# Kernel optimization log

Measured on AMD Instinct MI355X. Metric: run time of the kernel, lower is better.

The kernel has to match this reference:

```python
import jax, jax.numpy as jnp
import numpy as np

K = 16        # max_points
S = 3         # num_scales
D_MODEL = 256
KDIM = 16
TAU = 1e-4
B_BATCH = 512


def _boundaries(k):
    edges = [(i, j) for i in range(k) for j in range(i + 1, k)]
    tris = [(i, j, kk) for i in range(k) for j in range(i + 1, k) for kk in range(j + 1, k)]
    E, T = len(edges), len(tris)
    B1 = np.zeros((k, E), np.float32)
    for e, (i, j) in enumerate(edges):
        B1[i, e] = -1.0
        B1[j, e] = 1.0
    e2i = {e: idx for idx, e in enumerate(edges)}
    B2 = np.zeros((E, T), np.float32)
    for t, (i, j, kk) in enumerate(tris):
        B2[e2i[(j, kk)], t] = 1.0
        B2[e2i[(i, kk)], t] = -1.0
        B2[e2i[(i, j)], t] = 1.0
    e_i = np.array([e[0] for e in edges], np.int32)
    e_j = np.array([e[1] for e in edges], np.int32)
    t_ij = np.array([e2i[(a, b)] for (a, b, c) in tris], np.int32)
    t_jk = np.array([e2i[(b, c)] for (a, b, c) in tris], np.int32)
    t_ik = np.array([e2i[(a, c)] for (a, b, c) in tris], np.int32)
    return B1, B2, e_i, e_j, t_ij, t_jk, t_ik


def setup_inputs() -> dict:
    key = jax.random.key(0)
    ks = jax.random.split(key, 8)
    d = D_MODEL
    B1, B2, e_i, e_j, t_ij, t_jk, t_ik = _boundaries(K)

    def lin(kk, fin, fout):
        return jax.random.normal(kk, (fin, fout), jnp.float32) / np.sqrt(fin).astype(np.float32)

    return dict(
        x=jax.random.normal(ks[0], (B_BATCH, K, d), jnp.float32),
        mask=jnp.ones((B_BATCH, K), jnp.float32),
        B1=jnp.asarray(B1), B2=jnp.asarray(B2), abs_B1=jnp.asarray(np.abs(B1)),
        e_i=jnp.asarray(e_i), e_j=jnp.asarray(e_j),
        t_ij=jnp.asarray(t_ij), t_jk=jnp.asarray(t_jk), t_ik=jnp.asarray(t_ik),
        log_scales=jnp.linspace(-1.5, 1.5, S).astype(jnp.float32),
        Wg=lin(ks[1], d, KDIM), bg=jnp.zeros((KDIM,), jnp.float32),
        Wv0=lin(ks[2], d, d * S), bv0=jnp.zeros((d * S,), jnp.float32),
        We=lin(ks[3], d, d * S), be=jnp.zeros((d * S,), jnp.float32),
        Wout=lin(ks[4], 2 * S * d, d), bout=jnp.zeros((d,), jnp.float32),
        g1=jnp.ones((d,), jnp.float32), b1=jnp.zeros((d,), jnp.float32),
        g2=jnp.ones((d,), jnp.float32), b2=jnp.zeros((d,), jnp.float32),
        Wf1=lin(ks[5], d, 4 * d), bf1=jnp.zeros((4 * d,), jnp.float32),
        Wf2=lin(ks[6], 4 * d, d), bf2=jnp.zeros((d,), jnp.float32),
    )


def _layernorm(x, g, b):
    mu = jnp.mean(x, -1, keepdims=True)
    var = jnp.mean(jnp.square(x - mu), -1, keepdims=True)
    return (x - mu) * jax.lax.rsqrt(var + 1e-5) * g + b


def _forward(x, mask, B1, B2, abs_B1, e_i, e_j, t_ij, t_jk, t_ik,
             log_scales, Wg, bg, Wv0, bv0, We, be, Wout, bout,
             g1, b1, g2, b2, Wf1, bf1, Wf2, bf2):
    B, Kp, d = x.shape
    E = B1.shape[1]
    residual = x
    x_norm = _layernorm(x, g1, b1)
    P = x_norm @ Wg + bg                                   # (B,K,k_dim)
    mask2 = mask[:, :, None] * mask[:, None, :]            # (B,K,K)
    # cdist (safe sqrt: zero diag, no NaN grads)
    pn = jnp.sum(P * P, -1)
    d2 = jnp.maximum(pn[:, :, None] + pn[:, None, :] - 2.0 * jnp.einsum('bik,bjk->bij', P, P), 0.0)
    Dm = jnp.where(d2 > 0, jnp.sqrt(jnp.where(d2 > 0, d2, 1.0)), 0.0) * mask2
    sigma_sq = jnp.square(jnp.exp(log_scales))             # (S,)
    A = jnp.exp(-(Dm * Dm)[:, None] / (2.0 * sigma_sq[None, :, None, None] + 1e-8)) * mask2[:, None]  # (B,S,K,K)
    W1 = A[:, :, e_i, e_j]                                 # (B,S,E) edge gather
    W2 = W1[:, :, t_ij] * W1[:, :, t_jk] * W1[:, :, t_ik]  # (B,S,T) triangle weights
    V0 = (x_norm @ Wv0 + bv0).reshape(B, Kp, S, d).transpose(0, 2, 1, 3)         # (B,S,K,d)
    E_raw = jnp.einsum('ke,bkd->bed', abs_B1, x_norm)                            # (B,E,d)
    E_in = (E_raw @ We + be).reshape(B, E, S, d).transpose(0, 2, 1, 3)           # (B,S,E,d)
    # L0 = B1 diag(W1) B1^T + tau I
    L0 = jnp.einsum('ke,bse,me->bskm', B1, W1, B1) + TAU * jnp.eye(Kp, dtype=x.dtype)
    M0 = jnp.einsum('bskm,bsmd->bskd', L0, V0)
    # L1 = B1^T diag(mask) B1 + B2 diag(W2) B2^T + tau I
    term_down = jnp.einsum('ke,bk,kf->bef', B1, mask, B1)                        # (B,E,E)
    term_up = jnp.einsum('et,bst,ft->bsef', B2, W2, B2)                          # (B,S,E,E)
    L1 = term_down[:, None] + term_up + TAU * jnp.eye(E, dtype=x.dtype)
    M1 = jnp.einsum('bsef,bsfd->bsed', L1, E_in)
    M1n = jnp.einsum('ke,bsed->bskd', abs_B1, M1)                                # edges -> nodes
    node_cat = M0.transpose(0, 2, 1, 3).reshape(B, Kp, S * d)
    edge_cat = M1n.transpose(0, 2, 1, 3).reshape(B, Kp, S * d)
    attn = jnp.concatenate([node_cat, edge_cat], -1) @ Wout + bout
    x2 = residual + attn                                   # dropout is identity in eval
    h = jax.nn.gelu(_layernorm(x2, g2, b2) @ Wf1 + bf1, approximate=False) @ Wf2 + bf2
    return x2 + h


def reference(x, mask, B1, B2, abs_B1, e_i, e_j, t_ij, t_jk, t_ik,
              log_scales, Wg, bg, Wv0, bv0, We, be, Wout, bout,
              g1, b1, g2, b2, Wf1, bf1, Wf2, bf2):
    return _forward(x, mask, B1, B2, abs_B1, e_i, e_j, t_ij, t_jk, t_ik,
                    log_scales, Wg, bg, Wv0, bv0, We, be, Wout, bout,
                    g1, b1, g2, b2, Wf1, bf1, Wf2, bf2)
```

## Files before the change

kernel.cpp:

```cpp
#include <hip/hip_runtime.h>
#include <math.h>

#define KN 16
#define DM 256
#define NS 3
#define NE 120
#define NT_TRI 560
#define NBATCH 512
#define TAUF 1e-4f
#define KAUG 1664

typedef unsigned short ushort_t;
typedef __attribute__((ext_vector_type(8))) short short8v;
typedef __attribute__((ext_vector_type(4))) short short4v;
typedef __attribute__((ext_vector_type(4))) float f32x4;

#define OFF_WSTACK 0u
#define OFF_WF1T   851968u
#define OFF_WF2T   1376256u
#define OFF_TOPO   1900544u
#define OFF_RST    1908736u
#define OFF_TBF    2105344u
#define OFF_XNT    5251072u
#define OFF_Z      13639680u
#define OFF_H      13639680u

__device__ __forceinline__ ushort_t f2bf(float f) {
    union { float f; unsigned int u; } v; v.f = f;
    unsigned int r = v.u + 0x7FFFu + ((v.u >> 16) & 1u);
    return (ushort_t)(r >> 16);
}
__device__ __forceinline__ void gload_lds16(const void* g, void* l) {
    auto gp = (const __attribute__((address_space(1))) unsigned int*)(unsigned long long)(g);
    auto lp = (__attribute__((address_space(3))) unsigned int*)(unsigned long long)(l);
    __builtin_amdgcn_global_load_lds(gp, lp, 16, 0, 0);
}

__global__ __launch_bounds__(256) void prep_kernel(
    const float* __restrict__ Wv0, const float* __restrict__ bv0,
    const float* __restrict__ We,  const float* __restrict__ be,
    const float* __restrict__ Wout,
    const float* __restrict__ Wf1, const float* __restrict__ Wf2,
    const int* __restrict__ e_i, const int* __restrict__ e_j,
    const int* __restrict__ t_ij, const int* __restrict__ t_jk, const int* __restrict__ t_ik,
    ushort_t* __restrict__ wstack, ushort_t* __restrict__ wf1t,
    ushort_t* __restrict__ wf2t,
    float* __restrict__ topoF, int* __restrict__ midOff, int* __restrict__ triSrt)
{
    __shared__ float lhs[16][DM];
    __shared__ float tile[64][65];
    __shared__ int   eidxL[256];
    __shared__ int   eiL[NE], ejL[NE];
    __shared__ int   midL[NT_TRI], pkL[NT_TRI];
    __shared__ int   cnts[16], offs[17];
    const int bid = blockIdx.x;
    const int j = threadIdx.x;

    if (bid == 230) {
        eidxL[j] = -1;
        if (j < NE) { eiL[j] = e_i[j]; ejL[j] = e_j[j]; }
        __syncthreads();
        if (j < NE) {
            eidxL[eiL[j]*16 + ejL[j]] = j;
            eidxL[ejL[j]*16 + eiL[j]] = j;
        }
        __syncthreads();
        const int n = j >> 4, m = j & 15;
        float q, p2, adj;
        if (n != m) {
            const int e = eidxL[j];
            if (e >= 0) { q = (m == ejL[e]) ? 1.f : -1.f; p2 = 1.f; adj = 1.f; }
            else        { q = 0.f; p2 = 0.f; adj = 0.f; }
        } else {
            q = 0.f; p2 = 0.f; adj = 0.f;
            for (int kk = 0; kk < KN; ++kk) {
                if (kk == n) continue;
                const int e = eidxL[n*16 + kk];
                if (e >= 0) { q += (n == ejL[e]) ? 1.f : -1.f; p2 += 1.f; }
            }
        }
        topoF[j] = q; topoF[256 + j] = p2; topoF[512 + j] = adj;

        for (int tt = j; tt < NT_TRI; tt += 256) {
            const int eij = t_ij[tt], ejk = t_jk[tt], eik = t_ik[tt];
            const int a0 = eiL[eij], a1 = ejL[eij];
            const int b0 = eiL[ejk], b1v = ejL[ejk];
            const int c0 = eiL[eik], c1 = ejL[eik];
            const int mid = (b0 == a0 || b0 == a1) ? b0 : b1v;
            midL[tt] = mid;
            pkL[tt]  = (a0*16 + a1) | ((b0*16 + b1v) << 8) | ((c0*16 + c1) << 16);
        }
        __syncthreads();
        if (j < 16) {
            int c = 0;
            for (int tt = 0; tt < NT_TRI; ++tt) c += (midL[tt] == j);
            cnts[j] = c;
        }
        __syncthreads();
        if (j == 0) {
            int s = 0;
            for (int q2 = 0; q2 < 16; ++q2) { offs[q2] = s; s += cnts[q2]; }
            offs[16] = s;
        }
        __syncthreads();
        if (j < 17) midOff[j] = offs[j];
        for (int tt = j; tt < NT_TRI; tt += 256) {
            const int mid = midL[tt];
            int r = 0;
            for (int q2 = 0; q2 < NT_TRI; ++q2)
                r += (q2 < tt && midL[q2] == mid);
            triSrt[offs[mid] + r] = pkL[tt];
        }
        return;
    }

    if (bid < 102) {
        const int m = bid / 17, by = bid % 17;
        const int path = m / 3, s = m % 3;
        const float* __restrict__ Wo = Wout + (size_t)m*DM*DM;
        if (by == 16) {
            const float* bv = (path == 0) ? bv0 : be;
            const float f = (path == 0) ? 1.0f : 0.5f;
            float acc = 0.f;
            for (int k = 0; k < DM; ++k)
                acc += bv[s*DM + k] * f * Wo[k*DM + j];
            wstack[(size_t)j*KAUG + 1536 + m] = f2bf(acc);
            if (m == 0)
                for (int c = 1542; c < KAUG; ++c)
                    wstack[(size_t)j*KAUG + c] = 0;
            return;
        }
        const float* src = (path == 0) ? Wv0 : We;
        const int i0 = by * 16;
        for (int r = 0; r < 16; ++r)
            lhs[r][j] = src[(size_t)(i0 + r)*(NS*DM) + s*DM + j];
        __syncthreads();
        float acc[16];
#pragma unroll
        for (int r = 0; r < 16; ++r) acc[r] = 0.f;
        for (int k = 0; k < DM; ++k) {
            const float w = Wo[k*DM + j];
#pragma unroll
            for (int r = 0; r < 16; ++r) acc[r] += lhs[r][k] * w;
        }
#pragma unroll
        for (int r = 0; r < 16; ++r)
            wstack[(size_t)j*KAUG + m*DM + i0 + r] = f2bf(acc[r]);
        return;
    }

    const float* in; ushort_t* outp; int R, C, rt, ct;
    if (bid < 166) {
        const int q = bid - 102;
        in = Wf1; outp = wf1t; R = 256; C = 1024;
        rt = (q >> 4) * 64; ct = (q & 15) * 64;
    } else {
        const int q = bid - 166;
        in = Wf2; outp = wf2t; R = 1024; C = 256;
        rt = (q >> 2) * 64; ct = (q & 3) * 64;
    }
#pragma unroll
    for (int q2 = 0; q2 < 16; ++q2) {
        const int idx = q2*256 + j;
        const int r = idx >> 6, c = idx & 63;
        tile[r][c] = in[(size_t)(rt + r)*C + ct + c];
    }
    __syncthreads();
#pragma unroll
    for (int q2 = 0; q2 < 16; ++q2) {
        const int idx = q2*256 + j;
        const int cc = idx >> 6, rr = idx & 63;
        outp[(size_t)(ct + cc)*R + rt + rr] = f2bf(tile[rr][cc]);
    }
}

__global__ __launch_bounds__(256) void topo_kernel(
    const float* __restrict__ x, const float* __restrict__ mask,
    const float* __restrict__ log_scales,
    const float* __restrict__ Wg, const float* __restrict__ bg,
    const float* __restrict__ g1, const float* __restrict__ b1,
    const float* __restrict__ topoF, const int* __restrict__ midOff,
    const int* __restrict__ triSrt,
    ushort_t* __restrict__ tbf, ushort_t* __restrict__ xnt,
    float* __restrict__ rstOut)
{
    const int b = blockIdx.x;
    const int t = threadIdx.x;
    const int n = t >> 4, m = t & 15;

    __shared__ ushort_t xnbT[DM][32];
    __shared__ float Plds[KN][KN];
    __shared__ float mskL[KN];
    __shared__ float QL[256];
    __shared__ float P2L[256];
    __shared__ float adjL[256];
    __shared__ float sA[NS][KN][KN];
    __shared__ float part[4][NS][KN];
    __shared__ ushort_t Tbf[6][KN][32];

    QL[t]  = topoF[t];
    P2L[t] = topoF[256 + t];
    adjL[t] = topoF[512 + t];
    if (t < KN) mskL[t] = mask[b*KN + t];
    {
        const short8v z8 = {0,0,0,0,0,0,0,0};
        *(short8v*)&xnbT[t][16] = z8;
        *(short8v*)&xnbT[t][24] = z8;
    }

    float xv[16];
    {
        const int cg = m * 16;
        const float* xr = x + (size_t)(b*KN + n)*DM + cg;
        const f32x4 v0 = *(const f32x4*)(xr);
        const f32x4 v1 = *(const f32x4*)(xr + 4);
        const f32x4 v2 = *(const f32x4*)(xr + 8);
        const f32x4 v3 = *(const f32x4*)(xr + 12);
#pragma unroll
        for (int q = 0; q < 4; ++q) { xv[q] = v0[q]; xv[4+q] = v1[q]; xv[8+q] = v2[q]; xv[12+q] = v3[q]; }
        float ssum = 0.f;
#pragma unroll
        for (int q = 0; q < 16; ++q) ssum += xv[q];
#pragma unroll
        for (int o = 1; o < 16; o <<= 1) ssum += __shfl_xor(ssum, o);
        const float mu = ssum * (1.f/DM);
        float vsum = 0.f;
#pragma unroll
        for (int q = 0; q < 16; ++q) { const float d = xv[q]-mu; vsum += d*d; }
#pragma unroll
        for (int o = 1; o < 16; o <<= 1) vsum += __shfl_xor(vsum, o);
        const float rstd = rsqrtf(vsum*(1.f/DM) + 1e-5f);
        const f32x4 ga = *(const f32x4*)(g1 + cg),   gb = *(const f32x4*)(g1 + cg + 4);
        const f32x4 gc = *(const f32x4*)(g1 + cg + 8), gd = *(const f32x4*)(g1 + cg + 12);
        const f32x4 ba = *(const f32x4*)(b1 + cg),   bb = *(const f32x4*)(b1 + cg + 4);
        const f32x4 bc = *(const f32x4*)(b1 + cg + 8), bd = *(const f32x4*)(b1 + cg + 12);
        float gg[16], bbv[16];
#pragma unroll
        for (int q = 0; q < 4; ++q) {
            gg[q] = ga[q]; gg[4+q] = gb[q]; gg[8+q] = gc[q]; gg[12+q] = gd[q];
            bbv[q] = ba[q]; bbv[4+q] = bb[q]; bbv[8+q] = bc[q]; bbv[12+q] = bd[q];
        }
#pragma unroll
        for (int q = 0; q < 16; ++q) {
            xv[q] = (xv[q]-mu)*rstd*gg[q] + bbv[q];
            xnbT[cg + q][n] = f2bf(xv[q]);
        }
    }

    {
        float partc[16];
#pragma unroll
        for (int c = 0; c < 16; ++c) partc[c] = 0.f;
        const int cg = m * 16;
#pragma unroll
        for (int q = 0; q < 16; ++q) {
            const float xq = xv[q];
            const float* wr = Wg + (size_t)(cg + q)*KN;
            const f32x4 w0 = *(const f32x4*)(wr);
            const f32x4 w1 = *(const f32x4*)(wr + 4);
            const f32x4 w2 = *(const f32x4*)(wr + 8);
            const f32x4 w3 = *(const f32x4*)(wr + 12);
            partc[0]  += xq*w0[0]; partc[1]  += xq*w0[1]; partc[2]  += xq*w0[2]; partc[3]  += xq*w0[3];
            partc[4]  += xq*w1[0]; partc[5]  += xq*w1[1]; partc[6]  += xq*w1[2]; partc[7]  += xq*w1[3];
            partc[8]  += xq*w2[0]; partc[9]  += xq*w2[1]; partc[10] += xq*w2[2]; partc[11] += xq*w2[3];
            partc[12] += xq*w3[0]; partc[13] += xq*w3[1]; partc[14] += xq*w3[2]; partc[15] += xq*w3[3];
        }
        const int b0 = t & 1, b1b = (t>>1)&1, b2 = (t>>2)&1, b3 = (t>>3)&1;
        float p8[8];
#pragma unroll
        for (int c2 = 0; c2 < 8; ++c2) {
            const float keep = b0 ? partc[2*c2+1] : partc[2*c2];
            const float send = b0 ? partc[2*c2]   : partc[2*c2+1];
            p8[c2] = keep + __shfl_xor(send, 1);
        }
        float p4[4];
#pragma unroll
        for (int c2 = 0; c2 < 4; ++c2) {
            const float keep = b1b ? p8[2*c2+1] : p8[2*c2];
            const float send = b1b ? p8[2*c2]   : p8[2*c2+1];
            p4[c2] = keep + __shfl_xor(send, 2);
        }
        float p2v[2];
#pragma unroll
        for (int c2 = 0; c2 < 2; ++c2) {
            const float keep = b2 ? p4[2*c2+1] : p4[2*c2];
            const float send = b2 ? p4[2*c2]   : p4[2*c2+1];
            p2v[c2] = keep + __shfl_xor(send, 4);
        }
        const float keep = b3 ? p2v[1] : p2v[0];
        const float send = b3 ? p2v[0] : p2v[1];
        Plds[n][m] = keep + __shfl_xor(send, 8) + bg[m];
    }
    __syncthreads();

    float T0[NS], hq;
    {
        float d2 = 0.f;
#pragma unroll
        for (int k = 0; k < KN; ++k) {
            const float dd = Plds[n][k] - Plds[m][k];
            d2 += dd*dd;
        }
        const float m2v = mskL[n]*mskL[m];
        const float dm = (d2 > 0.f) ? sqrtf(d2)*m2v : 0.f;
        const float dmsq = dm*dm;
        const float adjv = adjL[t];
#pragma unroll
        for (int s = 0; s < NS; ++s) {
            const float sig2 = __expf(2.f*log_scales[s]);
            const float a = __expf(-dmsq/(2.f*sig2 + 1e-8f)) * m2v;
            sA[s][n][m] = a;
            const float am = a * adjv;
            float rsum = am;
#pragma unroll
            for (int o = 1; o < 16; o <<= 1) rsum += __shfl_xor(rsum, o);
            const float tv = (m == n) ? (TAUF + rsum) : (-am);
            T0[s] = tv;
            Tbf[s][n][m] = f2bf(tv);
        }
        hq = 0.f;
#pragma unroll
        for (int k = 0; k < KN; ++k)
            hq += mskL[k]*QL[n*16 + k]*QL[m*16 + k];
#pragma unroll
        for (int idx = 0; idx < 6; ++idx) {
            const int e2 = idx*256 + t;
            Tbf[e2 >> 8][(e2 >> 4) & 15][16 + (e2 & 15)] = 0;
        }
    }
    __syncthreads();

    {
        const int c4 = t >> 6, rem = t & 63;
        const int midb = rem & 15, sb = rem >> 4;
        if (sb < NS) {
            const float* sAf = &sA[sb][0][0];
            float acc = 0.f;
            const int lo = midOff[midb], hi = midOff[midb + 1];
            for (int ii = lo + c4; ii < hi; ii += 4) {
                const int pk = triSrt[ii];
                acc += sAf[pk & 255] * sAf[(pk >> 8) & 255] * sAf[(pk >> 16) & 255];
            }
            part[c4][sb][midb] = 4.f * acc;
        }
    }
    __syncthreads();

    {
        float T1[NS];
        const float p2v = P2L[t];
#pragma unroll
        for (int s = 0; s < NS; ++s) {
            float hup = 0.f;
            if (m == n)
                hup = part[0][s][n] + part[1][s][n] + part[2][s][n] + part[3][s][n];
            const float tv = hq + TAUF*p2v + hup;
            T1[s] = tv;
            Tbf[NS + s][n][m] = f2bf(tv);
        }
        float sv[6] = {T0[0], T0[1], T0[2], T1[0], T1[1], T1[2]};
#pragma unroll
        for (int q = 0; q < 6; ++q) {
            float v = sv[q];
#pragma unroll
            for (int o = 1; o < 16; o <<= 1) v += __shfl_xor(v, o);
            sv[q] = v;
        }
        const float wv = (m==0)?sv[0]:(m==1)?sv[1]:(m==2)?sv[2]:(m==3)?sv[3]:(m==4)?sv[4]:sv[5];
        if (m < 6) rstOut[(size_t)b*96 + m*16 + n] = wv;
    }
    __syncthreads();

    {
        const short8v* st = (const short8v*)&Tbf[0][0][0];
        short8v* dt = (short8v*)(tbf + (size_t)b*3072);
        dt[t] = st[t];
        if (t < 128) dt[256 + t] = st[256 + t];
        const short8v* sx = (const short8v*)&xnbT[0][0];
        short8v* dx = (short8v*)(xnt + (size_t)b*8192);
#pragma unroll
        for (int q = 0; q < 4; ++q) dx[q*256 + t] = sx[q*256 + t];
    }
}

__global__ __launch_bounds__(256) void zmfma_kernel(
    const ushort_t* __restrict__ tbf, const ushort_t* __restrict__ xnt,
    const float* __restrict__ rst, ushort_t* __restrict__ Z)
{
    const int b = blockIdx.x, t = threadIdx.x;
    __shared__ ushort_t xnbT[DM][32];
    __shared__ ushort_t Tbf[6][KN][32];
    __shared__ float rs[96];

    const ushort_t* xs = xnt + (size_t)b*8192;
    const ushort_t* ts = tbf + (size_t)b*3072;
#pragma unroll
    for (int q = 0; q < 4; ++q)
        gload_lds16(xs + (size_t)(q*256 + t)*8, ((ushort_t*)xnbT) + (q*256 + t)*8);
    gload_lds16(ts + (size_t)t*8, ((ushort_t*)Tbf) + t*8);
    if (t < 128)
        gload_lds16(ts + (size_t)(256 + t)*8, ((ushort_t*)Tbf) + (256 + t)*8);
    if (t < 96) rs[t] = rst[(size_t)b*96 + t];
    __syncthreads();

    ushort_t* Zb = Z + (size_t)b*KN*KAUG;
    const int w = t >> 6, l = t & 63;
    const int lr = l & 15, lk = l >> 4;
    short8v bfrT[6];
#pragma unroll
    for (int m6 = 0; m6 < 6; ++m6)
        bfrT[m6] = *(const short8v*)&Tbf[m6][lr][lk*8];
#pragma unroll
    for (int q4 = 0; q4 < 4; ++q4) {
        const int jb = w*64 + q4*16;
        const short8v axn = *(const short8v*)&xnbT[jb + lr][lk*8];
#pragma unroll
        for (int m6 = 0; m6 < 6; ++m6) {
            f32x4 acc = {0.f,0.f,0.f,0.f};
            acc = __builtin_amdgcn_mfma_f32_16x16x32_bf16(axn, bfrT[m6], acc, 0, 0, 0);
            short4v zv;
#pragma unroll
            for (int rg = 0; rg < 4; ++rg) zv[rg] = (short)f2bf(acc[rg]);
            *(short4v*)(Zb + (size_t)lr*KAUG + m6*256 + jb + lk*4) = zv;
        }
    }
    {
        const int row = t >> 4, grp = t & 15;
        short8v tv = {0,0,0,0,0,0,0,0};
        if (grp == 0) {
#pragma unroll
            for (int i = 0; i < 6; ++i) tv[i] = (short)f2bf(rs[i*16 + row]);
        }
        *(short8v*)(Zb + (size_t)row*KAUG + 1536 + grp*8) = tv;
    }
}

template<int BM, int BN, int BK, int KD, int EPI>
__global__ __launch_bounds__(256) void gemm_lds(
    const ushort_t* __restrict__ A, const ushort_t* __restrict__ Bt,
    const float* __restrict__ bias, const float* __restrict__ resid,
    float* __restrict__ outF, ushort_t* __restrict__ outH, int ldo)
{
    constexpr int ROWB = BK*2;
    constexpr int KS = BK/32;
    constexpr int MF = BM/32, NF = BN/32;
    constexpr int APASS = BM*ROWB/4096;
    constexpr int BPASS = BN*ROWB/4096;
    __shared__ ushort_t lA[BM*BK];
    __shared__ ushort_t lB[BN*BK];
    const int t = threadIdx.x;
    const int w = t >> 6, l = t & 63;
    const int wm = w & 1, wn = w >> 1;
    const int lr = l & 15, lk = l >> 4;
    const int brow = blockIdx.x * BM;
    const int bcol = blockIdx.y * BN;

    f32x4 acc[MF][NF];
#pragma unroll
    for (int mf = 0; mf < MF; ++mf)
#pragma unroll
        for (int nt = 0; nt < NF; ++nt)
            acc[mf][nt] = (f32x4){0.f,0.f,0.f,0.f};

    const int byteoff = t * 16;

    for (int kc = 0; kc < KD/BK; ++kc) {
        if (kc) __syncthreads();
#pragma unroll
        for (int c = 0; c < APASS; ++c) {
            const int bo = c*4096 + byteoff;
            const int row = bo / ROWB;
            const int gs = ((bo % ROWB) >> 4) ^ (row & 7);
            gload_lds16(A + (size_t)(brow + row)*KD + kc*BK + gs*8, lA + (bo >> 1));
        }
#pragma unroll
        for (int c = 0; c < BPASS; ++c) {
            const int bo = c*4096 + byteoff;
            const int row = bo / ROWB;
            const int gs = ((bo % ROWB) >> 4) ^ (row & 7);
            gload_lds16(Bt + (size_t)(bcol + row)*KD + kc*BK + gs*8, lB + (bo >> 1));
        }
        __syncthreads();
#pragma unroll
        for (int ks = 0; ks < KS; ++ks) {
            short8v af[MF], bfr[NF];
#pragma unroll
            for (int mf = 0; mf < MF; ++mf) {
                const int ra = wm*(BM/2) + mf*16 + lr;
                const int gs = (ks*4 + lk) ^ (ra & 7);
                af[mf] = *(const short8v*)(lA + ra*BK + gs*8);
            }
#pragma unroll
            for (int nt = 0; nt < NF; ++nt) {
                const int rb = wn*(BN/2) + nt*16 + lr;
                const int gs = (ks*4 + lk) ^ (rb & 7);
                bfr[nt] = *(const short8v*)(lB + rb*BK + gs*8);
            }
#pragma unroll
            for (int mf = 0; mf < MF; ++mf)
#pragma unroll
                for (int nt = 0; nt < NF; ++nt)
                    acc[mf][nt] = __builtin_amdgcn_mfma_f32_16x16x32_bf16(
                        af[mf], bfr[nt], acc[mf][nt], 0, 0, 0);
        }
    }

#pragma unroll
    for (int mf = 0; mf < MF; ++mf) {
#pragma unroll
        for (int nt = 0; nt < NF; ++nt) {
            const int col = bcol + wn*(BN/2) + nt*16 + lr;
#pragma unroll
            for (int rg = 0; rg < 4; ++rg) {
                const int row = brow + wm*(BM/2) + mf*16 + lk*4 + rg;
                const size_t o = (size_t)row * ldo + col;
                const float v = acc[mf][nt][rg];
                if (EPI == 2) {
                    outF[o] = outF[o] + v + bias[col];
                } else {
                    outF[o] = resid[o] + v + bias[col];
                }
            }
        }
    }
}

__global__ __launch_bounds__(256) void gemm_ffn1(
    const float* __restrict__ x2, const float* __restrict__ gv,
    const float* __restrict__ bv,
    const ushort_t* __restrict__ Bt, const float* __restrict__ bias,
    ushort_t* __restrict__ outH)
{
    constexpr int BM = 64, BN = 128, KD = 256, BK = 64, ROWB = BK*2;
    __shared__ ushort_t lnA[BM*KD];
    __shared__ ushort_t lB[BN*BK];
    const int t = threadIdx.x;
    const int w = t >> 6, l = t & 63;
    const int wm = w & 1, wn = w >> 1;
    const int lr = l & 15, lk = l >> 4;
    const int brow = blockIdx.x * BM;
    const int bcol = blockIdx.y * BN;

    {
        const int row = t >> 2, c0 = (t & 3) * 64;
        const float* xr = x2 + (size_t)(brow + row)*DM + c0;
        f32x4 va[16];
        float s = 0.f;
#pragma unroll
        for (int q = 0; q < 16; ++q) {
            va[q] = *(const f32x4*)(xr + q*4);
            s += va[q][0] + va[q][1] + va[q][2] + va[q][3];
        }
        s += __shfl_xor(s, 1); s += __shfl_xor(s, 2);
        const float mu = s * (1.f/DM);
        float vs = 0.f;
#pragma unroll
        for (int q = 0; q < 16; ++q) {
#pragma unroll
            for (int i = 0; i < 4; ++i) { const float d = va[q][i]-mu; vs += d*d; }
        }
        vs += __shfl_xor(vs, 1); vs += __shfl_xor(vs, 2);
        const float rstd = rsqrtf(vs*(1.f/DM) + 1e-5f);
#pragma unroll
        for (int q = 0; q < 16; q += 2) {
            short8v o;
#pragma unroll
            for (int i = 0; i < 4; ++i) {
                const int c = c0 + q*4 + i;
                o[i] = (short)f2bf((va[q][i]-mu)*rstd*gv[c] + bv[c]);
            }
#pragma unroll
            for (int i = 0; i < 4; ++i) {
                const int c = c0 + (q+1)*4 + i;
                o[4+i] = (short)f2bf((va[q+1][i]-mu)*rstd*gv[c] + bv[c]);
            }
            const int g = (c0 >> 3) + (q >> 1);
            const int gs = g ^ (row & 7);
            *(short8v*)(lnA + row*KD + gs*8) = o;
        }
    }

    f32x4 acc[2][4];
#pragma unroll
    for (int mf = 0; mf < 2; ++mf)
#pragma unroll
        for (int nt = 0; nt < 4; ++nt)
            acc[mf][nt] = (f32x4){0.f,0.f,0.f,0.f};

    const int byteoff = t * 16;
    for (int kc = 0; kc < KD/BK; ++kc) {
        __syncthreads();
#pragma unroll
        for (int c = 0; c < 4; ++c) {
            const int bo = c*4096 + byteoff;
            const int row = bo / ROWB;
            const int gs = ((bo % ROWB) >> 4) ^ (row & 7);
            gload_lds16(Bt + (size_t)(bcol + row)*KD + kc*BK + gs*8, lB + (bo >> 1));
        }
        __syncthreads();
#pragma unroll
        for (int ks = 0; ks < 2; ++ks) {
            short8v af[2], bfr[4];
#pragma unroll
            for (int mf = 0; mf < 2; ++mf) {
                const int ra = wm*32 + mf*16 + lr;
                const int g = kc*8 + ks*4 + lk;
                const int gs = g ^ (ra & 7);
                af[mf] = *(const short8v*)(lnA + ra*KD + gs*8);
            }
#pragma unroll
            for (int nt = 0; nt < 4; ++nt) {
                const int rb = wn*64 + nt*16 + lr;
                const int gs = (ks*4 + lk) ^ (rb & 7);
                bfr[nt] = *(const short8v*)(lB + rb*BK + gs*8);
            }
#pragma unroll
            for (int mf = 0; mf < 2; ++mf)
#pragma unroll
                for (int nt = 0; nt < 4; ++nt)
                    acc[mf][nt] = __builtin_amdgcn_mfma_f32_16x16x32_bf16(
                        af[mf], bfr[nt], acc[mf][nt], 0, 0, 0);
        }
    }

#pragma unroll
    for (int mf = 0; mf < 2; ++mf) {
#pragma unroll
        for (int nt = 0; nt < 4; ++nt) {
            const int col = bcol + wn*64 + nt*16 + lr;
#pragma unroll
            for (int rg = 0; rg < 4; ++rg) {
                const int row = brow + wm*32 + mf*16 + lk*4 + rg;
                const float u = acc[mf][nt][rg] + bias[col];
                const float a = 0.79788456080286536f*(u + 0.044715f*u*u*u);
                outH[(size_t)row*1024 + col] = f2bf(u / (1.f + __expf(-2.f*a)));
            }
        }
    }
}

extern "C" void kernel_launch(void* const* d_in, const int* in_sizes, int n_in,
                              void* d_out, int out_size, void* d_ws, size_t ws_size,
                              hipStream_t stream) {
    const float* x          = (const float*)d_in[0];
    const float* mask       = (const float*)d_in[1];
    const int*   e_i        = (const int*)  d_in[5];
    const int*   e_j        = (const int*)  d_in[6];
    const int*   t_ij       = (const int*)  d_in[7];
    const int*   t_jk       = (const int*)  d_in[8];
    const int*   t_ik       = (const int*)  d_in[9];
    const float* log_scales = (const float*)d_in[10];
    const float* Wg         = (const float*)d_in[11];
    const float* bg         = (const float*)d_in[12];
    const float* Wv0        = (const float*)d_in[13];
    const float* bv0        = (const float*)d_in[14];
    const float* We         = (const float*)d_in[15];
    const float* be         = (const float*)d_in[16];
    const float* Wout       = (const float*)d_in[17];
    const float* bout       = (const float*)d_in[18];
    const float* g1         = (const float*)d_in[19];
    const float* b1         = (const float*)d_in[20];
    const float* g2         = (const float*)d_in[21];
    const float* b2         = (const float*)d_in[22];
    const float* Wf1        = (const float*)d_in[23];
    const float* bf1        = (const float*)d_in[24];
    const float* Wf2        = (const float*)d_in[25];
    const float* bf2        = (const float*)d_in[26];

    char* wsb = (char*)d_ws;
    ushort_t* wstack = (ushort_t*)(wsb + OFF_WSTACK);
    ushort_t* wf1t   = (ushort_t*)(wsb + OFF_WF1T);
    ushort_t* wf2t   = (ushort_t*)(wsb + OFF_WF2T);
    float*    topoF  = (float*)   (wsb + OFF_TOPO);
    int*      midOff = (int*)     (wsb + OFF_TOPO + 3072);
    int*      triSrt = (int*)     (wsb + OFF_TOPO + 3200);
    float*    rst    = (float*)   (wsb + OFF_RST);
    ushort_t* tbf    = (ushort_t*)(wsb + OFF_TBF);
    ushort_t* xnt    = (ushort_t*)(wsb + OFF_XNT);
    ushort_t* Z      = (ushort_t*)(wsb + OFF_Z);
    ushort_t* H      = (ushort_t*)(wsb + OFF_H);
    float*    out    = (float*)d_out;

    hipLaunchKernelGGL(prep_kernel, dim3(231), dim3(256), 0, stream,
                       Wv0, bv0, We, be, Wout, Wf1, Wf2,
                       e_i, e_j, t_ij, t_jk, t_ik,
                       wstack, wf1t, wf2t, topoF, midOff, triSrt);
    hipLaunchKernelGGL(topo_kernel, dim3(NBATCH), dim3(256), 0, stream,
                       x, mask, log_scales, Wg, bg, g1, b1,
                       topoF, midOff, triSrt, tbf, xnt, rst);
    hipLaunchKernelGGL(zmfma_kernel, dim3(NBATCH), dim3(256), 0, stream,
                       tbf, xnt, rst, Z);
    hipLaunchKernelGGL((gemm_lds<64,64,128,KAUG,3>), dim3(128,4), dim3(256), 0, stream,
                       Z, wstack, bout, x, out, (ushort_t*)nullptr, 256);
    hipLaunchKernelGGL(gemm_ffn1, dim3(128,8), dim3(256), 0, stream,
                       out, g2, b2, wf1t, bf1, H);
    hipLaunchKernelGGL((gemm_lds<64,64,128,1024,2>), dim3(128,4), dim3(256), 0, stream,
                       H, wf2t, bf2, (const float*)nullptr,
                       out, (ushort_t*)nullptr, 256);
}
```

Baseline: 139.7 us.

## Fuse topology and Z-MFMA kernels, staging Z rows in shared memory

Measured after the change: 131.1 us. -6.1%, faster.

```diff
diff --git a/kernel.cpp b/kernel.cpp
--- a/kernel.cpp
+++ b/kernel.cpp
@@ -9,6 +9,7 @@
 #define NBATCH 512
 #define TAUF 1e-4f
 #define KAUG 1664
+#define ZPITCH 1672
 
 typedef unsigned short ushort_t;
 typedef __attribute__((ext_vector_type(8))) short short8v;
@@ -19,11 +20,8 @@
 #define OFF_WF1T   851968u
 #define OFF_WF2T   1376256u
 #define OFF_TOPO   1900544u
-#define OFF_RST    1908736u
-#define OFF_TBF    2105344u
-#define OFF_XNT    5251072u
-#define OFF_Z      13639680u
-#define OFF_H      13639680u
+#define OFF_Z      1908736u
+#define OFF_H      1908736u
 
 __device__ __forceinline__ ushort_t f2bf(float f) {
     union { float f; unsigned int u; } v; v.f = f;
@@ -174,38 +172,36 @@
     }
 }
 
-__global__ __launch_bounds__(256) void topo_kernel(
+__global__ __launch_bounds__(256) void topoz_kernel(
     const float* __restrict__ x, const float* __restrict__ mask,
     const float* __restrict__ log_scales,
     const float* __restrict__ Wg, const float* __restrict__ bg,
     const float* __restrict__ g1, const float* __restrict__ b1,
     const float* __restrict__ topoF, const int* __restrict__ midOff,
     const int* __restrict__ triSrt,
-    ushort_t* __restrict__ tbf, ushort_t* __restrict__ xnt,
-    float* __restrict__ rstOut)
+    ushort_t* __restrict__ Z)
 {
     const int b = blockIdx.x;
     const int t = threadIdx.x;
     const int n = t >> 4, m = t & 15;
 
-    __shared__ ushort_t xnbT[DM][32];
-    __shared__ float Plds[KN][KN];
-    __shared__ float mskL[KN];
-    __shared__ float QL[256];
-    __shared__ float P2L[256];
-    __shared__ float adjL[256];
-    __shared__ float sA[NS][KN][KN];
-    __shared__ float part[4][NS][KN];
-    __shared__ ushort_t Tbf[6][KN][32];
-
-    QL[t]  = topoF[t];
-    P2L[t] = topoF[256 + t];
-    adjL[t] = topoF[512 + t];
+    __shared__ ushort_t xnbT[DM][16];
+    __shared__ ushort_t Tbf[6][KN][16];
+    __shared__ ushort_t Zstage[KN][ZPITCH];
+    __shared__ float    Plds[KN][KN];
+    __shared__ float    sA[NS][KN*KN];
+    __shared__ float    mskL[KN];
+    __shared__ int      triL[NT_TRI];
+    float (*part)[NS][KN] = (float(*)[NS][KN])&Plds[0][0];
+
     if (t < KN) mskL[t] = mask[b*KN + t];
+    for (int idx = t; idx < NT_TRI; idx += 256) triL[idx] = triSrt[idx];
     {
         const short8v z8 = {0,0,0,0,0,0,0,0};
-        *(short8v*)&xnbT[t][16] = z8;
-        *(short8v*)&xnbT[t][24] = z8;
+        for (int i2 = t; i2 < 16*17; i2 += 256) {
+            const int row = i2 / 17, ch = i2 % 17;
+            *(short8v*)&Zstage[row][1536 + ch*8] = z8;
+        }
     }
 
     float xv[16];
@@ -304,12 +300,12 @@
         const float m2v = mskL[n]*mskL[m];
         const float dm = (d2 > 0.f) ? sqrtf(d2)*m2v : 0.f;
         const float dmsq = dm*dm;
-        const float adjv = adjL[t];
+        const float adjv = topoF[512 + t];
 #pragma unroll
         for (int s = 0; s < NS; ++s) {
             const float sig2 = __expf(2.f*log_scales[s]);
             const float a = __expf(-dmsq/(2.f*sig2 + 1e-8f)) * m2v;
-            sA[s][n][m] = a;
+            sA[s][t] = a;
             const float am = a * adjv;
             float rsum = am;
 #pragma unroll
@@ -321,12 +317,7 @@
         hq = 0.f;
 #pragma unroll
         for (int k = 0; k < KN; ++k)
-            hq += mskL[k]*QL[n*16 + k]*QL[m*16 + k];
-#pragma unroll
-        for (int idx = 0; idx < 6; ++idx) {
-            const int e2 = idx*256 + t;
-            Tbf[e2 >> 8][(e2 >> 4) & 15][16 + (e2 & 15)] = 0;
-        }
+            hq += mskL[k]*topoF[n*16 + k]*topoF[m*16 + k];
     }
     __syncthreads();
 
@@ -334,11 +325,11 @@
         const int c4 = t >> 6, rem = t & 63;
         const int midb = rem & 15, sb = rem >> 4;
         if (sb < NS) {
-            const float* sAf = &sA[sb][0][0];
+            const float* sAf = &sA[sb][0];
             float acc = 0.f;
             const int lo = midOff[midb], hi = midOff[midb + 1];
             for (int ii = lo + c4; ii < hi; ii += 4) {
-                const int pk = triSrt[ii];
+                const int pk = triL[ii];
                 acc += sAf[pk & 255] * sAf[(pk >> 8) & 255] * sAf[(pk >> 16) & 255];
             }
             part[c4][sb][midb] = 4.f * acc;
@@ -348,7 +339,7 @@
 
     {
         float T1[NS];
-        const float p2v = P2L[t];
+        const float p2v = topoF[256 + t];
 #pragma unroll
         for (int s = 0; s < NS; ++s) {
             float hup = 0.f;
@@ -367,71 +358,44 @@
             sv[q] = v;
         }
         const float wv = (m==0)?sv[0]:(m==1)?sv[1]:(m==2)?sv[2]:(m==3)?sv[3]:(m==4)?sv[4]:sv[5];
-        if (m < 6) rstOut[(size_t)b*96 + m*16 + n] = wv;
+        if (m < 6) Zstage[n][1536 + m] = f2bf(wv);
     }
     __syncthreads();
 
     {
-        const short8v* st = (const short8v*)&Tbf[0][0][0];
-        short8v* dt = (short8v*)(tbf + (size_t)b*3072);
-        dt[t] = st[t];
-        if (t < 128) dt[256 + t] = st[256 + t];
-        const short8v* sx = (const short8v*)&xnbT[0][0];
-        short8v* dx = (short8v*)(xnt + (size_t)b*8192);
-#pragma unroll
-        for (int q = 0; q < 4; ++q) dx[q*256 + t] = sx[q*256 + t];
-    }
-}
-
-__global__ __launch_bounds__(256) void zmfma_kernel(
-    const ushort_t* __restrict__ tbf, const ushort_t* __restrict__ xnt,
-    const float* __restrict__ rst, ushort_t* __restrict__ Z)
-{
-    const int b = blockIdx.x, t = threadIdx.x;
-    __shared__ ushort_t xnbT[DM][32];
-    __shared__ ushort_t Tbf[6][KN][32];
-    __shared__ float rs[96];
-
-    const ushort_t* xs = xnt + (size_t)b*8192;
-    const ushort_t* ts = tbf + (size_t)b*3072;
-#pragma unroll
-    for (int q = 0; q < 4; ++q)
-        gload_lds16(xs + (size_t)(q*256 + t)*8, ((ushort_t*)xnbT) + (q*256 + t)*8);
-    gload_lds16(ts + (size_t)t*8, ((ushort_t*)Tbf) + t*8);
-    if (t < 128)
-        gload_lds16(ts + (size_t)(256 + t)*8, ((ushort_t*)Tbf) + (256 + t)*8);
-    if (t < 96) rs[t] = rst[(size_t)b*96 + t];
+        const int w = t >> 6, l = t & 63;
+        const int lr = l & 15, lk = l >> 4;
+        const short8v z8 = {0,0,0,0,0,0,0,0};
+        short8v bfrT[6];
+#pragma unroll
+        for (int m6 = 0; m6 < 6; ++m6)
+            bfrT[m6] = (lk < 2) ? *(const short8v*)&Tbf[m6][lr][lk*8] : z8;
+#pragma unroll
+        for (int q4 = 0; q4 < 4; ++q4) {
+            const int jb = w*64 + q4*16;
+            const short8v axn = (lk < 2) ? *(const short8v*)&xnbT[jb + lr][lk*8] : z8;
+#pragma unroll
+            for (int m6 = 0; m6 < 6; ++m6) {
+                f32x4 acc = {0.f,0.f,0.f,0.f};
+                acc = __builtin_amdgcn_mfma_f32_16x16x32_bf16(axn, bfrT[m6], acc, 0, 0, 0);
+                short4v zv;
+#pragma unroll
+                for (int rg = 0; rg < 4; ++rg) zv[rg] = (short)f2bf(acc[rg]);
+                *(short4v*)&Zstage[lr][m6*256 + jb + lk*4] = zv;
+            }
+        }
+    }
     __syncthreads();
 
-    ushort_t* Zb = Z + (size_t)b*KN*KAUG;
-    const int w = t >> 6, l = t & 63;
-    const int lr = l & 15, lk = l >> 4;
-    short8v bfrT[6];
-#pragma unroll
-    for (int m6 = 0; m6 < 6; ++m6)
-        bfrT[m6] = *(const short8v*)&Tbf[m6][lr][lk*8];
-#pragma unroll
-    for (int q4 = 0; q4 < 4; ++q4) {
-        const int jb = w*64 + q4*16;
-        const short8v axn = *(const short8v*)&xnbT[jb + lr][lk*8];
-#pragma unroll
-        for (int m6 = 0; m6 < 6; ++m6) {
-            f32x4 acc = {0.f,0.f,0.f,0.f};
-            acc = __builtin_amdgcn_mfma_f32_16x16x32_bf16(axn, bfrT[m6], acc, 0, 0, 0);
-            short4v zv;
-#pragma unroll
-            for (int rg = 0; rg < 4; ++rg) zv[rg] = (short)f2bf(acc[rg]);
-            *(short4v*)(Zb + (size_t)lr*KAUG + m6*256 + jb + lk*4) = zv;
-        }
-    }
-    {
-        const int row = t >> 4, grp = t & 15;
-        short8v tv = {0,0,0,0,0,0,0,0};
-        if (grp == 0) {
-#pragma unroll
-            for (int i = 0; i < 6; ++i) tv[i] = (short)f2bf(rs[i*16 + row]);
-        }
-        *(short8v*)(Zb + (size_t)row*KAUG + 1536 + grp*8) = tv;
+    {
+        ushort_t* Zb = Z + (size_t)b*KN*KAUG;
+#pragma unroll
+        for (int i = 0; i < 13; ++i) {
+            const int cid = t + 256*i;
+            const int row = cid / 208;
+            const int off = (cid % 208) * 8;
+            *(short8v*)(Zb + (size_t)row*KAUG + off) = *(const short8v*)&Zstage[row][off];
+        }
     }
 }
 
@@ -674,9 +638,6 @@
     float*    topoF  = (float*)   (wsb + OFF_TOPO);
     int*      midOff = (int*)     (wsb + OFF_TOPO + 3072);
     int*      triSrt = (int*)     (wsb + OFF_TOPO + 3200);
-    float*    rst    = (float*)   (wsb + OFF_RST);
-    ushort_t* tbf    = (ushort_t*)(wsb + OFF_TBF);
-    ushort_t* xnt    = (ushort_t*)(wsb + OFF_XNT);
     ushort_t* Z      = (ushort_t*)(wsb + OFF_Z);
     ushort_t* H      = (ushort_t*)(wsb + OFF_H);
     float*    out    = (float*)d_out;
@@ -685,11 +646,9 @@
                        Wv0, bv0, We, be, Wout, Wf1, Wf2,
                        e_i, e_j, t_ij, t_jk, t_ik,
                        wstack, wf1t, wf2t, topoF, midOff, triSrt);
-    hipLaunchKernelGGL(topo_kernel, dim3(NBATCH), dim3(256), 0, stream,
+    hipLaunchKernelGGL(topoz_kernel, dim3(NBATCH), dim3(256), 0, stream,
                        x, mask, log_scales, Wg, bg, g1, b1,
-                       topoF, midOff, triSrt, tbf, xnt, rst);
-    hipLaunchKernelGGL(zmfma_kernel, dim3(NBATCH), dim3(256), 0, stream,
-                       tbf, xnt, rst, Z);
+                       topoF, midOff, triSrt, Z);
     hipLaunchKernelGGL((gemm_lds<64,64,128,KAUG,3>), dim3(128,4), dim3(256), 0, stream,
                        Z, wstack, bout, x, out, (ushort_t*)nullptr, 256);
     hipLaunchKernelGGL(gemm_ffn1, dim3(128,8), dim3(256), 0, stream,
```
